# Optimization experiments

Measured on AMD Instinct MI355X. Metric: run time of the kernel, lower is better.

The kernel has to match this reference:

```python
import jax, jax.numpy as jnp
import numpy as np

B, N, R = 8, 1024, 8192
D_IN, REL_D = 32, 1
NF_P, NF_R, NF_E, D_OUT = 128, 128, 128, 3
PSTEP = 3


def setup_inputs() -> dict:
    key = jax.random.key(0)
    ks = jax.random.split(key, 26)
    state = jax.random.normal(ks[0], (B, N, D_IN), dtype=jnp.float32)
    # Rr/Rs are one-hot selection matrices [B, N, R]: column j selects the
    # receiver/sender particle of relation j.
    recv = jax.random.randint(ks[1], (B, R), 0, N)
    send = jax.random.randint(ks[2], (B, R), 0, N)
    Rr = jnp.transpose(jax.nn.one_hot(recv, N, dtype=jnp.float32), (0, 2, 1))
    Rs = jnp.transpose(jax.nn.one_hot(send, N, dtype=jnp.float32), (0, 2, 1))
    Ra = jax.random.normal(ks[3], (B, R, REL_D), dtype=jnp.float32)

    def lin(k, i, o):
        kw, kb = jax.random.split(k)
        return (0.02 * jax.random.normal(kw, (i, o), dtype=jnp.float32),
                0.02 * jax.random.normal(kb, (o,), dtype=jnp.float32))

    pe_w0, pe_b0 = lin(ks[4], D_IN, NF_P)
    pe_w1, pe_b1 = lin(ks[5], NF_P, NF_E)
    re_w0, re_b0 = lin(ks[6], 2 * D_IN + REL_D, NF_R)
    re_w1, re_b1 = lin(ks[7], NF_R, NF_R)
    re_w2, re_b2 = lin(ks[8], NF_R, NF_R)
    rp_w, rp_b = lin(ks[9], NF_R + 2 * NF_E, NF_E)   # relation_propagator
    pp_w, pp_b = lin(ks[10], 2 * NF_E, NF_E)          # particle_propagator
    pr_w0, pr_b0 = lin(ks[11], NF_E, NF_E)            # particle_predictor
    pr_w1, pr_b1 = lin(ks[12], NF_E, D_OUT)
    return dict(state=state, Rr=Rr, Rs=Rs, Ra=Ra, pstep=PSTEP,
                pe_w0=pe_w0, pe_b0=pe_b0, pe_w1=pe_w1, pe_b1=pe_b1,
                re_w0=re_w0, re_b0=re_b0, re_w1=re_w1, re_b1=re_b1,
                re_w2=re_w2, re_b2=re_b2, rp_w=rp_w, rp_b=rp_b,
                pp_w=pp_w, pp_b=pp_b, pr_w0=pr_w0, pr_b0=pr_b0,
                pr_w1=pr_w1, pr_b1=pr_b1)


def reference(state, Rr, Rs, Ra, pstep,
              pe_w0, pe_b0, pe_w1, pe_b1,
              re_w0, re_b0, re_w1, re_b1, re_w2, re_b2,
              rp_w, rp_b, pp_w, pp_b,
              pr_w0, pr_b0, pr_w1, pr_b1):
    relu = jax.nn.relu
    # gather particle states into relation slots: Rr^T @ state -> [B, R, D]
    state_r = jnp.einsum('bnr,bnd->brd', Rr, state)
    state_s = jnp.einsum('bnr,bnd->brd', Rs, state)
    # particle encoder: Linear-ReLU-Linear-ReLU
    particle_encode = relu(relu(state @ pe_w0 + pe_b0) @ pe_w1 + pe_b1)  # [B,N,NF_E]
    # relation encoder: 3-layer MLP with ReLU after each layer
    rel_in = jnp.concatenate([state_r, state_s, Ra], axis=2)
    h = relu(rel_in @ re_w0 + re_b0)
    h = relu(h @ re_w1 + re_b1)
    relation_encode = relu(h @ re_w2 + re_b2)  # [B,R,NF_R]

    particle_effect = jnp.zeros((B, N, NF_E), dtype=state.dtype)
    for _ in range(pstep):
        effect_r = jnp.einsum('bnr,bne->bre', Rr, particle_effect)  # gather
        effect_s = jnp.einsum('bnr,bne->bre', Rs, particle_effect)
        rel_x = jnp.concatenate([relation_encode, effect_r, effect_s], axis=2)
        relation_effect = relu(rel_x @ rp_w + rp_b)  # [B,R,NF_E]
        # scatter-add relation effects back to receiver particles
        effect_agg = jnp.einsum('bnr,bre->bne', Rr, relation_effect)
        part_x = jnp.concatenate([particle_encode, effect_agg], axis=2)
        # residual particle propagator: relu(linear(x) + prev_effect)
        particle_effect = relu(part_x @ pp_w + pp_b + particle_effect)
    pred = relu(particle_effect @ pr_w0 + pr_b0) @ pr_w1 + pr_b1  # [B,N,D_OUT]
    return pred
```

## Files before the change

kernel.cpp:

```cpp
#include <hip/hip_runtime.h>

#define NB 8
#define NP 1024
#define NR 8192

typedef unsigned short u16;
typedef __attribute__((ext_vector_type(8))) short bf16x8;
typedef __attribute__((ext_vector_type(4))) float f32x4;

#define MFMA __builtin_amdgcn_mfma_f32_16x16x32_bf16

static __device__ __forceinline__ float bf2f(u16 u) {
    union { unsigned int i; float f; } v; v.i = ((unsigned int)u) << 16; return v.f;
}
static __device__ __forceinline__ unsigned int f2bf(float f) {
    union { float fv; unsigned int i; } v; v.fv = f;
    unsigned int r = v.i + 0x7FFFu + ((v.i >> 16) & 1u);
    return r >> 16;
}
static __device__ __forceinline__ unsigned int pack2(float a, float b) {
    return f2bf(a) | (f2bf(b) << 16);
}
static __device__ __forceinline__ void unpk8(uint4 v, float* o) {
    o[0] = bf2f((u16)(v.x & 0xFFFF)); o[1] = bf2f((u16)(v.x >> 16));
    o[2] = bf2f((u16)(v.y & 0xFFFF)); o[3] = bf2f((u16)(v.y >> 16));
    o[4] = bf2f((u16)(v.z & 0xFFFF)); o[5] = bf2f((u16)(v.z >> 16));
    o[6] = bf2f((u16)(v.w & 0xFFFF)); o[7] = bf2f((u16)(v.w >> 16));
}

__global__ __launch_bounds__(256) void k_indices(
    const uint4* __restrict__ Rr4, const uint4* __restrict__ Rs4,
    u16* __restrict__ recv, u16* __restrict__ send)
{
    long i = (long)blockIdx.x * 256 + threadIdx.x;
    int c4 = (int)(i & 2047);
    int n  = (int)((i >> 11) & 1023);
    int b  = (int)(i >> 21);
    int base = b * NR + c4 * 4;
    uint4 vr = Rr4[i];
    uint4 vs = Rs4[i];
    if (vr.x) recv[base + 0] = (u16)n;
    if (vr.y) recv[base + 1] = (u16)n;
    if (vr.z) recv[base + 2] = (u16)n;
    if (vr.w) recv[base + 3] = (u16)n;
    if (vs.x) send[base + 0] = (u16)n;
    if (vs.y) send[base + 1] = (u16)n;
    if (vs.z) send[base + 2] = (u16)n;
    if (vs.w) send[base + 3] = (u16)n;
}

__global__ __launch_bounds__(1024) void k_csr(
    const u16* __restrict__ recv, int* __restrict__ row_ptr,
    u16* __restrict__ rel_idx)
{
    __shared__ int s[NP];
    __shared__ int cur[NP];
    int b = blockIdx.x, t = threadIdx.x;
    cur[t] = 0;
    __syncthreads();
    int pv[NR / 1024];
    #pragma unroll
    for (int k = 0; k < NR / 1024; ++k) {
        pv[k] = recv[b * NR + k * 1024 + t] & 1023;
        atomicAdd(&cur[pv[k]], 1);
    }
    __syncthreads();
    int v = cur[t];
    s[t] = v;
    __syncthreads();
    #pragma unroll
    for (int off = 1; off < NP; off <<= 1) {
        int add = (t >= off) ? s[t - off] : 0;
        __syncthreads();
        s[t] += add;
        __syncthreads();
    }
    int excl = s[t] - v;
    row_ptr[b * (NP + 1) + t] = excl;
    cur[t] = excl;
    if (t == NP - 1) row_ptr[b * (NP + 1) + NP] = s[t];
    __syncthreads();
    #pragma unroll
    for (int k = 0; k < NR / 1024; ++k) {
        int pos = atomicAdd(&cur[pv[k]], 1) & 8191;
        rel_idx[b * NR + pos] = (u16)(k * 1024 + t);
    }
}

__global__ __launch_bounds__(256) void k_prep(
    const float* __restrict__ w0, const float* __restrict__ w1,
    const float* __restrict__ w2, const float* __restrict__ w3,
    const float* __restrict__ w4, const float* __restrict__ w5,
    const float* __restrict__ w6, const float* __restrict__ w7,
    bf16x8* __restrict__ out)
{
    const float* W; int KC, kv, off;
    switch (blockIdx.x) {
        case 0:  W = w0; KC = 3;  kv = 65;  off = 0;  break;
        case 1:  W = w1; KC = 4;  kv = 128; off = 6;  break;
        case 2:  W = w2; KC = 4;  kv = 128; off = 14; break;
        case 3:  W = w3; KC = 1;  kv = 32;  off = 22; break;
        case 4:  W = w4; KC = 4;  kv = 128; off = 24; break;
        case 5:  W = w5; KC = 12; kv = 384; off = 32; break;
        case 6:  W = w6; KC = 8;  kv = 256; off = 56; break;
        default: W = w7; KC = 4;  kv = 128; off = 72; break;
    }
    int tid = threadIdx.x;
    int wave = tid >> 6, quad = (tid >> 4) & 3, l16 = tid & 15;
    for (int kc = 0; kc < KC; ++kc)
      for (int nt = 0; nt < 2; ++nt) {
        bf16x8 f;
        #pragma unroll
        for (int j = 0; j < 8; ++j) {
            int k = kc*32 + quad*8 + j;
            f[j] = (k < kv) ? (short)f2bf(W[k*128 + wave*32 + nt*16 + l16]) : (short)0;
        }
        out[(off + kc*2 + nt)*256 + tid] = f;
      }
}

template<int KC>
static __device__ __forceinline__ void load_wfrag(
    const bf16x8* __restrict__ fb, bf16x8 (&wf)[KC][2], int tid)
{
    #pragma unroll
    for (int kc = 0; kc < KC; ++kc)
      #pragma unroll
      for (int nt = 0; nt < 2; ++nt)
        wf[kc][nt] = fb[(kc*2 + nt)*256 + tid];
}

template<int MT, int KC, int LDA>
static __device__ __forceinline__ void mfma_compute(
    const u16* xlds, const bf16x8 (&wf)[KC][2], f32x4 (&acc)[MT][2],
    int l16, int quad)
{
    #pragma unroll
    for (int kc = 0; kc < KC; ++kc) {
        bf16x8 a[MT];
        #pragma unroll
        for (int mt = 0; mt < MT; ++mt)
            a[mt] = *(const bf16x8*)(xlds + (mt*16 + l16)*LDA + kc*32 + quad*8);
        #pragma unroll
        for (int mt = 0; mt < MT; ++mt) {
            acc[mt][0] = MFMA(a[mt], wf[kc][0], acc[mt][0], 0, 0, 0);
            acc[mt][1] = MFMA(a[mt], wf[kc][1], acc[mt][1], 0, 0, 0);
        }
    }
}

template<int MT>
static __device__ __forceinline__ void zero_acc(f32x4 (&acc)[MT][2]) {
    #pragma unroll
    for (int mt = 0; mt < MT; ++mt)
      #pragma unroll
      for (int nt = 0; nt < 2; ++nt)
        acc[mt][nt] = f32x4{0.f, 0.f, 0.f, 0.f};
}

template<int MT, int LDA>
static __device__ __forceinline__ void store_c_lds(
    u16* xlds, const f32x4 (&acc)[MT][2], const float* __restrict__ bias,
    int wave, int quad, int l16, int coloff = 0)
{
    #pragma unroll
    for (int mt = 0; mt < MT; ++mt)
      #pragma unroll
      for (int nt = 0; nt < 2; ++nt) {
        int col = wave*32 + nt*16 + l16;
        float bv = bias[col];
        #pragma unroll
        for (int rg = 0; rg < 4; ++rg)
            xlds[(mt*16 + quad*4 + rg)*LDA + coloff + col] =
                (u16)f2bf(fmaxf(acc[mt][nt][rg] + bv, 0.f));
      }
}

template<int MT, bool RELU>
static __device__ __forceinline__ void store_c_glob(
    u16* __restrict__ out, long row0, const f32x4 (&acc)[MT][2],
    const float* __restrict__ bias, int wave, int quad, int l16)
{
    #pragma unroll
    for (int mt = 0; mt < MT; ++mt)
      #pragma unroll
      for (int nt = 0; nt < 2; ++nt) {
        int col = wave*32 + nt*16 + l16;
        float bv = bias[col];
        #pragma unroll
        for (int rg = 0; rg < 4; ++rg) {
            long r = row0 + mt*16 + quad*4 + rg;
            float v = acc[mt][nt][rg] + bv;
            if (RELU) v = fmaxf(v, 0.f);
            out[r*128 + col] = (u16)f2bf(v);
        }
      }
}

__global__ __launch_bounds__(256) void k_encpe(
    const float* __restrict__ state, const float* __restrict__ Ra,
    const u16* __restrict__ recv, const u16* __restrict__ send,
    const bf16x8* __restrict__ f_re0, const float* __restrict__ re_b0,
    const bf16x8* __restrict__ f_re1, const float* __restrict__ re_b1,
    const bf16x8* __restrict__ f_re2, const float* __restrict__ re_b2,
    const bf16x8* __restrict__ f_rpP, const float* __restrict__ rp_b,
    u16* __restrict__ bufP,
    const bf16x8* __restrict__ f_pe0, const float* __restrict__ pe_b0,
    const bf16x8* __restrict__ f_pe1, const float* __restrict__ pe_b1,
    u16* __restrict__ penc)
{
    constexpr int LDA = 136;
    __shared__ __align__(16) u16 xlds[64 * LDA];
    const int tid = threadIdx.x;
    const int wave = tid >> 6, quad = (tid >> 4) & 3, l16 = tid & 15;
    f32x4 acc[4][2];

    if (blockIdx.x < 1024) {
        const int row0 = blockIdx.x * 64;
        const int b = row0 >> 13;
        {
            int r = tid >> 2, tt = tid & 3;
            int rel = row0 + r;
            u16* dst = xlds + r * LDA;
            int ri = recv[rel] & 1023;
            int si = send[rel] & 1023;
            const float* rrow = state + ((long)(b*NP + ri)) * 32;
            const float* srow = state + ((long)(b*NP + si)) * 32;
            float4 a0 = *(const float4*)(rrow + tt*8);
            float4 a1 = *(const float4*)(rrow + tt*8 + 4);
            uint4 o;
            o.x = pack2(a0.x, a0.y); o.y = pack2(a0.z, a0.w);
            o.z = pack2(a1.x, a1.y); o.w = pack2(a1.z, a1.w);
            *(uint4*)(dst + tt*8) = o;
            float4 s0 = *(const float4*)(srow + tt*8);
            float4 s1 = *(const float4*)(srow + tt*8 + 4);
            o.x = pack2(s0.x, s0.y); o.y = pack2(s0.z, s0.w);
            o.z = pack2(s1.x, s1.y); o.w = pack2(s1.z, s1.w);
            *(uint4*)(dst + 32 + tt*8) = o;
            if (tt == 3) {
                uint4 z = make_uint4(0, 0, 0, 0);
                *(uint4*)(dst + 64) = z; *(uint4*)(dst + 72) = z;
                *(uint4*)(dst + 80) = z; *(uint4*)(dst + 88) = z;
                dst[64] = (u16)f2bf(Ra[rel]);
            }
        }
        __syncthreads();
        zero_acc<4>(acc);
        {
            bf16x8 wf[3][2];
            load_wfrag<3>(f_re0, wf, tid);
            mfma_compute<4, 3, LDA>(xlds, wf, acc, l16, quad);
        }
        __syncthreads();
        store_c_lds<4, LDA>(xlds, acc, re_b0, wave, quad, l16);
        __syncthreads();
        zero_acc<4>(acc);
        {
            bf16x8 wf[4][2];
            load_wfrag<4>(f_re1, wf, tid);
            mfma_compute<4, 4, LDA>(xlds, wf, acc, l16, quad);
        }
        __syncthreads();
        store_c_lds<4, LDA>(xlds, acc, re_b1, wave, quad, l16);
        __syncthreads();
        zero_acc<4>(acc);
        {
            bf16x8 wf[4][2];
            load_wfrag<4>(f_re2, wf, tid);
            mfma_compute<4, 4, LDA>(xlds, wf, acc, l16, quad);
        }
        __syncthreads();
        store_c_lds<4, LDA>(xlds, acc, re_b2, wave, quad, l16);
        __syncthreads();
        zero_acc<4>(acc);
        {
            bf16x8 wf[4][2];
            load_wfrag<4>(f_rpP, wf, tid);
            mfma_compute<4, 4, LDA>(xlds, wf, acc, l16, quad);
        }
        store_c_glob<4, false>(bufP, row0, acc, rp_b, wave, quad, l16);
    } else {
        const long row0 = (long)(blockIdx.x - 1024) * 64;
        for (int idx = tid; idx < 64 * 8; idx += 256) {
            int r = idx >> 3, c = idx & 7;
            float4 v = *(const float4*)(state + (row0 + r)*32 + c*4);
            uint2 o; o.x = pack2(v.x, v.y); o.y = pack2(v.z, v.w);
            *(uint2*)(xlds + r*LDA + c*4) = o;
        }
        __syncthreads();
        zero_acc<4>(acc);
        {
            bf16x8 wf[1][2];
            load_wfrag<1>(f_pe0, wf, tid);
            mfma_compute<4, 1, LDA>(xlds, wf, acc, l16, quad);
        }
        __syncthreads();
        store_c_lds<4, LDA>(xlds, acc, pe_b0, wave, quad, l16);
        __syncthreads();
        zero_acc<4>(acc);
        {
            bf16x8 wf[4][2];
            load_wfrag<4>(f_pe1, wf, tid);
            mfma_compute<4, 4, LDA>(xlds, wf, acc, l16, quad);
        }
        store_c_glob<4, true>(penc, row0, acc, pe_b1, wave, quad, l16);
    }
}

template<bool STEP1, bool MAKEUV, bool LAST>
__global__ __launch_bounds__(256) void k_pp(
    const u16* __restrict__ penc, const u16* __restrict__ bufP,
    const u16* __restrict__ UV_in, u16* __restrict__ UV_out,
    const int* __restrict__ row_ptr, const u16* __restrict__ rel_idx,
    const u16* __restrict__ send,
    const bf16x8* __restrict__ f_pp, const float* __restrict__ pp_b,
    const bf16x8* __restrict__ f_U, const bf16x8* __restrict__ f_V,
    const bf16x8* __restrict__ f_pr0, const float* __restrict__ pr_b0,
    const float* __restrict__ pr_w1, const float* __restrict__ pr_b1,
    float* __restrict__ peff32_io, float* __restrict__ out)
{
    constexpr int LDA = 264;
    __shared__ __align__(16) u16 xlds[32 * LDA];
    const int tid = threadIdx.x;
    const int wave = tid >> 6, quad = (tid >> 4) & 3, l16 = tid & 15;
    const long row0 = (long)blockIdx.x * 32;

    for (int idx = tid; idx < 512; idx += 256) {
        int r = idx >> 4, c = idx & 15;
        *(uint4*)(xlds + r*LDA + c*8) = *(const uint4*)(penc + (row0 + r)*128 + c*8);
    }
    {
        int pp = tid >> 3;
        int cq = tid & 7;
        int gp = (int)row0 + pp;
        int b = gp >> 10, pl = gp & 1023;
        const int* rp = row_ptr + b * (NP + 1);
        int s0 = rp[pl], e0 = rp[pl + 1];
        float a[16];
        #pragma unroll
        for (int t = 0; t < 16; ++t) a[t] = 0.f;
        float uv[16];
        if (!STEP1) {
            const u16* ur = UV_in + ((long)gp)*256 + cq*16;
            unpk8(*(const uint4*)ur, uv);
            unpk8(*(const uint4*)(ur + 8), uv + 8);
        }
        for (int j = s0; j < e0; ++j) {
            int rel = rel_idx[b * NR + j] & 8191;
            const u16* prow = bufP + ((long)(b * NR + rel))*128 + cq*16;
            float pv[16];
            unpk8(*(const uint4*)prow, pv);
            unpk8(*(const uint4*)(prow + 8), pv + 8);
            if (STEP1) {
                #pragma unroll
                for (int e = 0; e < 16; ++e) a[e] += fmaxf(pv[e], 0.f);
            } else {
                int sj = send[b * NR + rel] & 1023;
                const u16* vrow = UV_in + ((long)(b*NP + sj))*256 + 128 + cq*16;
                float vv[16];
                unpk8(*(const uint4*)vrow, vv);
                unpk8(*(const uint4*)(vrow + 8), vv + 8);
                #pragma unroll
                for (int e = 0; e < 16; ++e)
                    a[e] += fmaxf(pv[e] + uv[e] + vv[e], 0.f);
            }
        }
        u16* dst = xlds + pp*LDA + 128 + cq*16;
        uint4 o;
        o.x = pack2(a[0], a[1]);   o.y = pack2(a[2], a[3]);
        o.z = pack2(a[4], a[5]);   o.w = pack2(a[6], a[7]);
        *(uint4*)dst = o;
        o.x = pack2(a[8], a[9]);   o.y = pack2(a[10], a[11]);
        o.z = pack2(a[12], a[13]); o.w = pack2(a[14], a[15]);
        *(uint4*)(dst + 8) = o;
    }
    __syncthreads();

    f32x4 acc[2][2];
    {
        bf16x8 wf[8][2];
        load_wfrag<8>(f_pp, wf, tid);
        zero_acc<2>(acc);
        mfma_compute<2, 8, LDA>(xlds, wf, acc, l16, quad);
    }
    __syncthreads();

    #pragma unroll
    for (int mt = 0; mt < 2; ++mt)
      #pragma unroll
      for (int nt = 0; nt < 2; ++nt) {
        int col = wave*32 + nt*16 + l16;
        float bv = pp_b[col];
        #pragma unroll
        for (int rg = 0; rg < 4; ++rg) {
            int rloc = mt*16 + quad*4 + rg;
            long r = row0 + rloc;
            float prev = STEP1 ? 0.f : peff32_io[r*128 + col];
            float v = fmaxf(acc[mt][nt][rg] + bv + prev, 0.f);
            if (!LAST) peff32_io[r*128 + col] = v;
            xlds[rloc*LDA + col] = (u16)f2bf(v);
        }
      }
    __syncthreads();

    if (MAKEUV) {
        #pragma unroll
        for (int half = 0; half < 2; ++half) {
            bf16x8 wf[4][2];
            load_wfrag<4>(half ? f_V : f_U, wf, tid);
            zero_acc<2>(acc);
            mfma_compute<2, 4, LDA>(xlds, wf, acc, l16, quad);
            #pragma unroll
            for (int mt = 0; mt < 2; ++mt)
              #pragma unroll
              for (int nt = 0; nt < 2; ++nt) {
                int col = half*128 + wave*32 + nt*16 + l16;
                #pragma unroll
                for (int rg = 0; rg < 4; ++rg) {
                    long r = row0 + mt*16 + quad*4 + rg;
                    UV_out[r*256 + col] = (u16)f2bf(acc[mt][nt][rg]);
                }
              }
        }
    }
    if (LAST) {
        bf16x8 wf[4][2];
        load_wfrag<4>(f_pr0, wf, tid);
        zero_acc<2>(acc);
        mfma_compute<2, 4, LDA>(xlds, wf, acc, l16, quad);
        store_c_lds<2, LDA>(xlds, acc, pr_b0, wave, quad, l16, 128);
        __syncthreads();
        if (tid < 96) {
            int row = tid / 3, col = tid - row * 3;
            float s = pr_b1[col];
            const u16* hr = xlds + row * LDA + 128;
            #pragma unroll 8
            for (int k = 0; k < 128; ++k) s += bf2f(hr[k]) * pr_w1[k*3 + col];
            out[(row0 + row)*3 + col] = s;
        }
    }
}

extern "C" void kernel_launch(void* const* d_in, const int* in_sizes, int n_in,
                              void* d_out, int out_size, void* d_ws, size_t ws_size,
                              hipStream_t stream) {
    const float* state = (const float*)d_in[0];
    const float* Rr    = (const float*)d_in[1];
    const float* Rs    = (const float*)d_in[2];
    const float* Ra    = (const float*)d_in[3];
    const float* pe_w0 = (const float*)d_in[5];
    const float* pe_b0 = (const float*)d_in[6];
    const float* pe_w1 = (const float*)d_in[7];
    const float* pe_b1 = (const float*)d_in[8];
    const float* re_w0 = (const float*)d_in[9];
    const float* re_b0 = (const float*)d_in[10];
    const float* re_w1 = (const float*)d_in[11];
    const float* re_b1 = (const float*)d_in[12];
    const float* re_w2 = (const float*)d_in[13];
    const float* re_b2 = (const float*)d_in[14];
    const float* rp_w  = (const float*)d_in[15];
    const float* rp_b  = (const float*)d_in[16];
    const float* pp_w  = (const float*)d_in[17];
    const float* pp_b  = (const float*)d_in[18];
    const float* pr_w0 = (const float*)d_in[19];
    const float* pr_b0 = (const float*)d_in[20];
    const float* pr_w1 = (const float*)d_in[21];
    const float* pr_b1 = (const float*)d_in[22];

    char* p = (char*)d_ws;
    u16*    bufP    = (u16*)p;    p += (size_t)NB*NR*128*2;
    u16*    UVa     = (u16*)p;    p += (size_t)NB*NP*256*2;
    u16*    UVb     = (u16*)p;    p += (size_t)NB*NP*256*2;
    float*  peff32  = (float*)p;  p += (size_t)NB*NP*128*4;
    u16*    penc    = (u16*)p;    p += (size_t)NB*NP*128*2;
    bf16x8* wfrag   = (bf16x8*)p; p += (size_t)80*256*16;
    int*    row_ptr = (int*)p;    p += (size_t)NB*(NP+1)*4 + 12;
    u16*    recv    = (u16*)p;    p += (size_t)NB*NR*2;
    u16*    send    = (u16*)p;    p += (size_t)NB*NR*2;
    u16*    rel_idx = (u16*)p;    p += (size_t)NB*NR*2;

    const bf16x8* f_re0 = wfrag + 0*256;
    const bf16x8* f_re1 = wfrag + 6*256;
    const bf16x8* f_re2 = wfrag + 14*256;
    const bf16x8* f_pe0 = wfrag + 22*256;
    const bf16x8* f_pe1 = wfrag + 24*256;
    const bf16x8* f_rpP = wfrag + 32*256;
    const bf16x8* f_rpU = wfrag + 40*256;
    const bf16x8* f_rpV = wfrag + 48*256;
    const bf16x8* f_pp  = wfrag + 56*256;
    const bf16x8* f_pr0 = wfrag + 72*256;

    float* outp = (float*)d_out;

    k_prep<<<8, 256, 0, stream>>>(re_w0, re_w1, re_w2, pe_w0, pe_w1, rp_w, pp_w, pr_w0, wfrag);
    k_indices<<<65536, 256, 0, stream>>>((const uint4*)Rr, (const uint4*)Rs, recv, send);
    k_csr<<<NB, 1024, 0, stream>>>(recv, row_ptr, rel_idx);
    k_encpe<<<1152, 256, 0, stream>>>(state, Ra, recv, send,
                                      f_re0, re_b0, f_re1, re_b1, f_re2, re_b2,
                                      f_rpP, rp_b, bufP,
                                      f_pe0, pe_b0, f_pe1, pe_b1, penc);
    k_pp<true,  true,  false><<<256, 256, 0, stream>>>(
        penc, bufP, UVa, UVa, row_ptr, rel_idx, send, f_pp, pp_b,
        f_rpU, f_rpV, f_pr0, pr_b0, pr_w1, pr_b1, peff32, outp);
    k_pp<false, true,  false><<<256, 256, 0, stream>>>(
        penc, bufP, UVa, UVb, row_ptr, rel_idx, send, f_pp, pp_b,
        f_rpU, f_rpV, f_pr0, pr_b0, pr_w1, pr_b1, peff32, outp);
    k_pp<false, false, true><<<256, 256, 0, stream>>>(
        penc, bufP, UVb, UVa, row_ptr, rel_idx, send, f_pp, pp_b,
        f_rpU, f_rpV, f_pr0, pr_b0, pr_w1, pr_b1, peff32, outp);
}
```

Measured before the change: 674.3 us.

## Store relation encodings in receiver-sorted order and merge prep into index kernel

New measurement: 646.1 us. 4.2% less time.

```diff
diff --git a/kernel.cpp b/kernel.cpp
--- a/kernel.cpp
+++ b/kernel.cpp
@@ -28,11 +28,42 @@
     o[6] = bf2f((u16)(v.w & 0xFFFF)); o[7] = bf2f((u16)(v.w >> 16));
 }
 
-__global__ __launch_bounds__(256) void k_indices(
+__global__ __launch_bounds__(256) void k_idxprep(
     const uint4* __restrict__ Rr4, const uint4* __restrict__ Rs4,
-    u16* __restrict__ recv, u16* __restrict__ send)
-{
-    long i = (long)blockIdx.x * 256 + threadIdx.x;
+    u16* __restrict__ recv, u16* __restrict__ send,
+    const float* __restrict__ w0, const float* __restrict__ w1,
+    const float* __restrict__ w2, const float* __restrict__ w3,
+    const float* __restrict__ w4, const float* __restrict__ w5,
+    const float* __restrict__ w6, const float* __restrict__ w7,
+    bf16x8* __restrict__ wfrag)
+{
+    int tid = threadIdx.x;
+    if (blockIdx.x < 8) {
+        const float* W; int KC, kv, off;
+        switch (blockIdx.x) {
+            case 0:  W = w0; KC = 3;  kv = 65;  off = 0;  break;
+            case 1:  W = w1; KC = 4;  kv = 128; off = 6;  break;
+            case 2:  W = w2; KC = 4;  kv = 128; off = 14; break;
+            case 3:  W = w3; KC = 1;  kv = 32;  off = 22; break;
+            case 4:  W = w4; KC = 4;  kv = 128; off = 24; break;
+            case 5:  W = w5; KC = 12; kv = 384; off = 32; break;
+            case 6:  W = w6; KC = 8;  kv = 256; off = 56; break;
+            default: W = w7; KC = 4;  kv = 128; off = 72; break;
+        }
+        int wave = tid >> 6, quad = (tid >> 4) & 3, l16 = tid & 15;
+        for (int kc = 0; kc < KC; ++kc)
+          for (int nt = 0; nt < 2; ++nt) {
+            bf16x8 f;
+            #pragma unroll
+            for (int j = 0; j < 8; ++j) {
+                int k = kc*32 + quad*8 + j;
+                f[j] = (k < kv) ? (short)f2bf(W[k*128 + wave*32 + nt*16 + l16]) : (short)0;
+            }
+            wfrag[(off + kc*2 + nt)*256 + tid] = f;
+          }
+        return;
+    }
+    long i = (long)(blockIdx.x - 8) * 256 + tid;
     int c4 = (int)(i & 2047);
     int n  = (int)((i >> 11) & 1023);
     int b  = (int)(i >> 21);
@@ -50,8 +81,9 @@
 }
 
 __global__ __launch_bounds__(1024) void k_csr(
-    const u16* __restrict__ recv, int* __restrict__ row_ptr,
-    u16* __restrict__ rel_idx)
+    const u16* __restrict__ recv, const u16* __restrict__ send,
+    int* __restrict__ row_ptr, u16* __restrict__ pos,
+    u16* __restrict__ send_sorted)
 {
     __shared__ int s[NP];
     __shared__ int cur[NP];
@@ -82,41 +114,11 @@
     __syncthreads();
     #pragma unroll
     for (int k = 0; k < NR / 1024; ++k) {
-        int pos = atomicAdd(&cur[pv[k]], 1) & 8191;
-        rel_idx[b * NR + pos] = (u16)(k * 1024 + t);
-    }
-}
-
-__global__ __launch_bounds__(256) void k_prep(
-    const float* __restrict__ w0, const float* __restrict__ w1,
-    const float* __restrict__ w2, const float* __restrict__ w3,
-    const float* __restrict__ w4, const float* __restrict__ w5,
-    const float* __restrict__ w6, const float* __restrict__ w7,
-    bf16x8* __restrict__ out)
-{
-    const float* W; int KC, kv, off;
-    switch (blockIdx.x) {
-        case 0:  W = w0; KC = 3;  kv = 65;  off = 0;  break;
-        case 1:  W = w1; KC = 4;  kv = 128; off = 6;  break;
-        case 2:  W = w2; KC = 4;  kv = 128; off = 14; break;
-        case 3:  W = w3; KC = 1;  kv = 32;  off = 22; break;
-        case 4:  W = w4; KC = 4;  kv = 128; off = 24; break;
-        case 5:  W = w5; KC = 12; kv = 384; off = 32; break;
-        case 6:  W = w6; KC = 8;  kv = 256; off = 56; break;
-        default: W = w7; KC = 4;  kv = 128; off = 72; break;
-    }
-    int tid = threadIdx.x;
-    int wave = tid >> 6, quad = (tid >> 4) & 3, l16 = tid & 15;
-    for (int kc = 0; kc < KC; ++kc)
-      for (int nt = 0; nt < 2; ++nt) {
-        bf16x8 f;
-        #pragma unroll
-        for (int j = 0; j < 8; ++j) {
-            int k = kc*32 + quad*8 + j;
-            f[j] = (k < kv) ? (short)f2bf(W[k*128 + wave*32 + nt*16 + l16]) : (short)0;
-        }
-        out[(off + kc*2 + nt)*256 + tid] = f;
-      }
+        int r = k * 1024 + t;
+        int j = atomicAdd(&cur[pv[k]], 1) & 8191;
+        pos[b * NR + r] = (u16)j;
+        send_sorted[b * NR + j] = send[b * NR + r];
+    }
 }
 
 template<int KC>
@@ -200,6 +202,7 @@
 __global__ __launch_bounds__(256) void k_encpe(
     const float* __restrict__ state, const float* __restrict__ Ra,
     const u16* __restrict__ recv, const u16* __restrict__ send,
+    const u16* __restrict__ pos,
     const bf16x8* __restrict__ f_re0, const float* __restrict__ re_b0,
     const bf16x8* __restrict__ f_re1, const float* __restrict__ re_b1,
     const bf16x8* __restrict__ f_re2, const float* __restrict__ re_b2,
@@ -278,7 +281,19 @@
             load_wfrag<4>(f_rpP, wf, tid);
             mfma_compute<4, 4, LDA>(xlds, wf, acc, l16, quad);
         }
-        store_c_glob<4, false>(bufP, row0, acc, rp_b, wave, quad, l16);
+        #pragma unroll
+        for (int mt = 0; mt < 4; ++mt)
+          #pragma unroll
+          for (int nt = 0; nt < 2; ++nt) {
+            int col = wave*32 + nt*16 + l16;
+            float bv = rp_b[col];
+            #pragma unroll
+            for (int rg = 0; rg < 4; ++rg) {
+                int rl = mt*16 + quad*4 + rg;
+                int j = pos[row0 + rl] & 8191;
+                bufP[((long)(b*NR + j))*128 + col] = (u16)f2bf(acc[mt][nt][rg] + bv);
+            }
+          }
     } else {
         const long row0 = (long)(blockIdx.x - 1024) * 64;
         for (int idx = tid; idx < 64 * 8; idx += 256) {
@@ -311,8 +326,7 @@
 __global__ __launch_bounds__(256) void k_pp(
     const u16* __restrict__ penc, const u16* __restrict__ bufP,
     const u16* __restrict__ UV_in, u16* __restrict__ UV_out,
-    const int* __restrict__ row_ptr, const u16* __restrict__ rel_idx,
-    const u16* __restrict__ send,
+    const int* __restrict__ row_ptr, const u16* __restrict__ send_sorted,
     const bf16x8* __restrict__ f_pp, const float* __restrict__ pp_b,
     const bf16x8* __restrict__ f_U, const bf16x8* __restrict__ f_V,
     const bf16x8* __restrict__ f_pr0, const float* __restrict__ pr_b0,
@@ -346,8 +360,7 @@
             unpk8(*(const uint4*)(ur + 8), uv + 8);
         }
         for (int j = s0; j < e0; ++j) {
-            int rel = rel_idx[b * NR + j] & 8191;
-            const u16* prow = bufP + ((long)(b * NR + rel))*128 + cq*16;
+            const u16* prow = bufP + ((long)(b*NR + j))*128 + cq*16;
             float pv[16];
             unpk8(*(const uint4*)prow, pv);
             unpk8(*(const uint4*)(prow + 8), pv + 8);
@@ -355,7 +368,7 @@
                 #pragma unroll
                 for (int e = 0; e < 16; ++e) a[e] += fmaxf(pv[e], 0.f);
             } else {
-                int sj = send[b * NR + rel] & 1023;
+                int sj = send_sorted[b * NR + j] & 1023;
                 const u16* vrow = UV_in + ((long)(b*NP + sj))*256 + 128 + cq*16;
                 float vv[16];
                 unpk8(*(const uint4*)vrow, vv);
@@ -477,7 +490,8 @@
     int*    row_ptr = (int*)p;    p += (size_t)NB*(NP+1)*4 + 12;
     u16*    recv    = (u16*)p;    p += (size_t)NB*NR*2;
     u16*    send    = (u16*)p;    p += (size_t)NB*NR*2;
-    u16*    rel_idx = (u16*)p;    p += (size_t)NB*NR*2;
+    u16*    pos     = (u16*)p;    p += (size_t)NB*NR*2;
+    u16*    send_s  = (u16*)p;    p += (size_t)NB*NR*2;
 
     const bf16x8* f_re0 = wfrag + 0*256;
     const bf16x8* f_re1 = wfrag + 6*256;
@@ -492,20 +506,21 @@
 
     float* outp = (float*)d_out;
 
-    k_prep<<<8, 256, 0, stream>>>(re_w0, re_w1, re_w2, pe_w0, pe_w1, rp_w, pp_w, pr_w0, wfrag);
-    k_indices<<<65536, 256, 0, stream>>>((const uint4*)Rr, (const uint4*)Rs, recv, send);
-    k_csr<<<NB, 1024, 0, stream>>>(recv, row_ptr, rel_idx);
-    k_encpe<<<1152, 256, 0, stream>>>(state, Ra, recv, send,
+    k_idxprep<<<65544, 256, 0, stream>>>((const uint4*)Rr, (const uint4*)Rs, recv, send,
+                                         re_w0, re_w1, re_w2, pe_w0, pe_w1, rp_w, pp_w, pr_w0,
+                                         wfrag);
+    k_csr<<<NB, 1024, 0, stream>>>(recv, send, row_ptr, pos, send_s);
+    k_encpe<<<1152, 256, 0, stream>>>(state, Ra, recv, send, pos,
                                       f_re0, re_b0, f_re1, re_b1, f_re2, re_b2,
                                       f_rpP, rp_b, bufP,
                                       f_pe0, pe_b0, f_pe1, pe_b1, penc);
     k_pp<true,  true,  false><<<256, 256, 0, stream>>>(
-        penc, bufP, UVa, UVa, row_ptr, rel_idx, send, f_pp, pp_b,
+        penc, bufP, UVa, UVa, row_ptr, send_s, f_pp, pp_b,
         f_rpU, f_rpV, f_pr0, pr_b0, pr_w1, pr_b1, peff32, outp);
     k_pp<false, true,  false><<<256, 256, 0, stream>>>(
-        penc, bufP, UVa, UVb, row_ptr, rel_idx, send, f_pp, pp_b,
+        penc, bufP, UVa, UVb, row_ptr, send_s, f_pp, pp_b,
         f_rpU, f_rpV, f_pr0, pr_b0, pr_w1, pr_b1, peff32, outp);
     k_pp<false, false, true><<<256, 256, 0, stream>>>(
-        penc, bufP, UVb, UVa, row_ptr, rel_idx, send, f_pp, pp_b,
+        penc, bufP, UVb, UVa, row_ptr, send_s, f_pp, pp_b,
         f_rpU, f_rpV, f_pr0, pr_b0, pr_w1, pr_b1, peff32, outp);
 }
```
